# Optimization experiments

Measured on AMD Instinct MI355X. Metric: run time of the kernel, lower is better.

Reference implementation:

```python
import jax, jax.numpy as jnp
import numpy as np

RAD2DEG = 180.0 / 3.14159  # module uses 3.14159, not pi

def _conv2d(x, w):
    # x: (N,1,H,W), w: (O,1,3,3), SAME padding, stride 1
    return jax.lax.conv_general_dilated(
        x, w, window_strides=(1, 1), padding='SAME',
        dimension_numbers=('NCHW', 'OIHW', 'NCHW'))

def _make_filters():
    sobel = np.array([[1, 0, -1], [2, 0, -2], [1, 0, -1]], dtype=np.float32)
    f0   = [[0,0,0],[0,1,-1],[0,0,0]]
    f45  = [[0,0,0],[0,1,0],[0,0,-1]]
    f90  = [[0,0,0],[0,1,0],[0,-1,0]]
    f135 = [[0,0,0],[0,1,0],[-1,0,0]]
    f180 = [[0,0,0],[-1,1,0],[0,0,0]]
    f225 = [[-1,0,0],[0,1,0],[0,0,0]]
    f270 = [[0,-1,0],[0,1,0],[0,0,0]]
    f315 = [[0,0,-1],[0,1,0],[0,0,0]]
    dirs = np.stack([f0,f45,f90,f135,f180,f225,f270,f315]).astype(np.float32)
    return sobel, dirs

def setup_inputs() -> dict:
    key = jax.random.key(0)
    H, W = 2160, 3840
    img = jax.random.uniform(key, (1, 3, H, W), dtype=jnp.float32)
    sobel, dirs = _make_filters()
    sobel_h = jnp.asarray(sobel)[None, None]          # (1,1,3,3)
    sobel_v = jnp.asarray(sobel.T)[None, None]        # (1,1,3,3)
    dir_w = jnp.asarray(dirs)[:, None]                # (8,1,3,3)
    return {"img": img, "sobel_h": sobel_h, "sobel_v": sobel_v, "dir_w": dir_w}

def reference(img, sobel_h, sobel_v, dir_w):
    # grayscale: mean of the 3 channels
    gray = (img[:, 0:1] + img[:, 1:2] + img[:, 2:3]) / 3.0        # (1,1,H,W)
    grad_x = _conv2d(gray, sobel_h)
    grad_y = _conv2d(gray, sobel_v)
    grad_mag = jnp.sqrt(grad_x ** 2 + grad_y ** 2)                # (1,1,H,W)
    # orientation in degrees, snapped to multiples of 45 (round-half-even, like torch.round)
    ori = jnp.round((jnp.arctan2(grad_y, grad_x) * RAD2DEG + 180.0) / 45.0)
    idx_pos = jnp.mod(ori, 8.0).astype(jnp.int32)                 # (1,1,H,W)
    idx_neg = jnp.mod(ori + 4.0, 8.0).astype(jnp.int32)
    all_filtered = _conv2d(grad_mag, dir_w)                       # (1,8,H,W)
    # per-pixel channel select (the flattened gather in the original)
    pos = jnp.take_along_axis(all_filtered, idx_pos, axis=1)      # (1,1,H,W)
    neg = jnp.take_along_axis(all_filtered, idx_neg, axis=1)
    is_max = jnp.minimum(pos, neg) > 0.0
    # in-place aliasing in the original: thin_edges/early_threshold alias grad_mag,
    # so the final binary map is: is_max AND (grad_mag >= 0.2)
    th = jnp.where(is_max & (grad_mag >= 0.2), 1.0, 0.0).astype(jnp.float32)
    return th
```

## Files before the change

kernel.cpp:

```cpp
#include <hip/hip_runtime.h>
#include <math.h>

#define IMG_W 3840
#define IMG_H 2160
#define OUTW  60
#define R     20
#define GROWS (R + 4)
#define MROWS (R + 2)

#define DXPACK 0x901A
#define DYPACK 0x1A9

#define T1_SLOPE 0.41421317376456f
#define T2_SLOPE 2.41420676743300f
#define SECT_EPS 3.0e-5f

__device__ __noinline__ int slow_sector(float sx, float sy) {
#pragma clang fp contract(off)
    const float RADF = (float)(180.0 / 3.14159);
    float t = atan2f(sy, sx);
    float wv = ((t * RADF) + 180.0f) / 45.0f;
    float ori = rintf(wv);
    float fr = fabsf(wv - ori);
    if (fr > 0.4995f) {
        double td = atan2((double)sy, (double)sx);
        float t2 = (float)td;
        wv = ((t2 * RADF) + 180.0f) / 45.0f;
        ori = rintf(wv);
    }
    return ((int)ori) & 7;
}

__global__ __launch_bounds__(256, 4) void canny_like_kernel(const float* __restrict__ img,
                                                            float* __restrict__ out) {
#pragma clang fp contract(off)
    __shared__ float lds_m[4][4][64];

    const int lane = threadIdx.x;
    const int w    = threadIdx.y;
    const int X0   = (blockIdx.x * 4 + w) * OUTW;
    const int Y0   = blockIdx.y * R;
    const int x    = X0 - 2 + lane;
    const bool xok    = (unsigned)x < (unsigned)IMG_W;
    const int  xc     = min(max(x, 0), IMG_W - 1);
    const bool xmok   = (lane >= 1) && (lane <= 62) && xok;
    const bool xoutok = (lane >= 2) && (lane <= 61);

    const float* im1 = img + (size_t)IMG_W * IMG_H;
    const float* im2 = img + 2 * (size_t)IMG_W * IMG_H;

    float g[GROWS];
#pragma unroll
    for (int k = 0; k < GROWS; ++k) {
        const int  y   = Y0 - 2 + k;
        const bool yok = (unsigned)y < (unsigned)IMG_H;
        const int  yc  = min(max(y, 0), IMG_H - 1);
        const int  o   = yc * IMG_W + xc;
        float c0 = img[o], c1 = im1[o], c2 = im2[o];
        float t = ((c0 + c1) + c2) / 3.0f;
        g[k] = (xok && yok) ? t : 0.0f;
    }

    float* const B = &lds_m[w][0][0];

    float gl[3], gr[3];
    gl[0] = __shfl_up(g[0], 1);  gr[0] = __shfl_down(g[0], 1);
    gl[1] = __shfl_up(g[1], 1);  gr[1] = __shfl_down(g[1], 1);

    float mc_p  = 0.0f;
    int   off_p = 0;

#pragma unroll
    for (int m = 0; m < MROWS; ++m) {
        const int i0 = m % 3, i1 = (m + 1) % 3, i2 = (m + 2) % 3;
        gl[i2] = __shfl_up(g[m + 2], 1);
        gr[i2] = __shfl_down(g[m + 2], 1);

        float a00 = gl[i0], a01 = g[m],     a02 = gr[i0];
        float a10 = gl[i1],                 a12 = gr[i1];
        float a20 = gl[i2], a21 = g[m + 2], a22 = gr[i2];
        float sx = a00;
        sx = sx - a02;
        sx = sx + 2.0f * a10;
        sx = sx - 2.0f * a12;
        sx = sx + a20;
        sx = sx - a22;
        float sy = a00;
        sy = sy + 2.0f * a01;
        sy = sy + a02;
        sy = sy - a20;
        sy = sy - 2.0f * a21;
        sy = sy - a22;
        float magv = sqrtf(sx * sx + sy * sy);

        float ax = fabsf(sx), ay = fabsf(sy);
        float d1 = fmaf(-T1_SLOPE, ax, ay);
        float d2 = fmaf(-T2_SLOPE, ax, ay);
        float sA = ax + ay;
        int dxo, dyo;
        if (__builtin_expect(fabsf(d1) < SECT_EPS * sA || fabsf(d2) < SECT_EPS * sA, 0)) {
            int idx = slow_sector(sx, sy);
            dxo = ((DXPACK >> (2 * idx)) & 3) - 1;
            dyo = ((DYPACK >> (2 * idx)) & 3) - 1;
        } else {
            dxo = (d2 > 0.0f) ? 0 : ((sx > 0.0f) ? -1 : 1);
            dyo = (d1 < 0.0f) ? 0 : ((sy > 0.0f) ? -1 : 1);
        }
        const bool vok = xmok && ((unsigned)(Y0 - 1 + m) < (unsigned)IMG_H);
        float mag  = vok ? magv : 0.0f;
        int   offv = vok ? (dyo * 64 + dxo) : 0;

        B[(m & 3) * 64 + lane] = mag;

        if (m >= 2) {
            const int rp  = ((m - 1) & 3) * 64;
            const int ipp = (rp + lane + off_p) & 255;
            const int ipn = (rp + lane - off_p) & 255;
            float mp = B[ipp];
            float mn = B[ipn];
            float res = (fminf(mc_p - mp, mc_p - mn) > 0.0f && mc_p >= 0.2f) ? 1.0f : 0.0f;
            if (xoutok)
                out[(size_t)(Y0 + m - 2) * IMG_W + x] = res;
        }
        mc_p  = mag;
        off_p = offv;
    }
}

extern "C" void kernel_launch(void* const* d_in, const int* in_sizes, int n_in,
                              void* d_out, int out_size, void* d_ws, size_t ws_size,
                              hipStream_t stream) {
    const float* img = (const float*)d_in[0];
    float* out = (float*)d_out;
    dim3 grid(64 / 4, IMG_H / R);
    dim3 block(64, 4);
    canny_like_kernel<<<grid, block, 0, stream>>>(img, out);
}
```

Baseline: 164.6 us.

## Stream image rows through a rolling 4-row register window with prefetch

Replaces the up-front load of all 24 grayscale rows into registers with a software-pipelined rolling window. Each iteration loads the three channels for row k+3 while computing gray, Sobel and NMS for earlier rows, and the loop is kept rolled in blocks of four. This cuts the large register footprint, which may allow higher occupancy. In exchange, each wave has fewer loads in flight, and a few extra clamped rows past the tile end are loaded and never used.

```diff
diff --git a/kernel.cpp b/kernel.cpp
--- a/kernel.cpp
+++ b/kernel.cpp
@@ -6,7 +6,6 @@
 #define OUTW  60
 #define R     20
 #define GROWS (R + 4)
-#define MROWS (R + 2)
 
 #define DXPACK 0x901A
 #define DYPACK 0x1A9
@@ -31,6 +30,81 @@
     return ((int)ori) & 7;
 }
 
+
+#define LOADROW(kk, cj)                                                        \
+    {                                                                          \
+        const int y_  = Y0 - 2 + (kk);                                         \
+        const int yc_ = min(max(y_, 0), IMG_H - 1);                            \
+        const int o_  = yc_ * IMG_W + xc;                                      \
+        c0[(cj)] = img[o_];                                                    \
+        c1[(cj)] = im1[o_];                                                    \
+        c2[(cj)] = im2[o_];                                                    \
+    }
+
+#define GRAY(kk, j3)                                                           \
+    {                                                                          \
+        const int  y_   = Y0 - 2 + (kk);                                       \
+        const bool yok_ = (unsigned)y_ < (unsigned)IMG_H;                      \
+        float t_  = ((c0[(j3)] + c1[(j3)]) + c2[(j3)]) / 3.0f;                 \
+        float gv_ = (xok && yok_) ? t_ : 0.0f;                                 \
+        g[(j3)]  = gv_;                                                        \
+        gl[(j3)] = __shfl_up(gv_, 1);                                          \
+        gr[(j3)] = __shfl_down(gv_, 1);                                        \
+    }
+
+#define MAGROW(kk, j3, DONMS)                                                  \
+    {                                                                          \
+        const int i0_ = ((j3) + 2) & 3, i1_ = ((j3) + 3) & 3, i2_ = (j3);      \
+        float a00 = gl[i0_], a01 = g[i0_], a02 = gr[i0_];                      \
+        float a10 = gl[i1_],               a12 = gr[i1_];                      \
+        float a20 = gl[i2_], a21 = g[i2_], a22 = gr[i2_];                      \
+        float sx = a00;                                \
+        sx = sx - a02;                                                         \
+        sx = sx + 2.0f * a10;                                                  \
+        sx = sx - 2.0f * a12;                                                  \
+        sx = sx + a20;                                                         \
+        sx = sx - a22;                                                         \
+        float sy = a00;                                                        \
+        sy = sy + 2.0f * a01;                                                  \
+        sy = sy + a02;                                                         \
+        sy = sy - a20;                                                         \
+        sy = sy - 2.0f * a21;                                                  \
+        sy = sy - a22;                                                         \
+        float magv = sqrtf(sx * sx + sy * sy);                                 \
+        float ax = fabsf(sx), ay = fabsf(sy);                                  \
+        float d1 = fmaf(-T1_SLOPE, ax, ay);                                    \
+        float d2 = fmaf(-T2_SLOPE, ax, ay);                                    \
+        float sA = ax + ay;                                                    \
+        int dxo, dyo;                                                          \
+        if (__builtin_expect(fabsf(d1) < SECT_EPS * sA ||                      \
+                             fabsf(d2) < SECT_EPS * sA, 0)) {                  \
+            int idx = slow_sector(sx, sy);                                     \
+            dxo = ((DXPACK >> (2 * idx)) & 3) - 1;                             \
+            dyo = ((DYPACK >> (2 * idx)) & 3) - 1;                             \
+        } else {                                                               \
+            dxo = (d2 > 0.0f) ? 0 : ((sx > 0.0f) ? -1 : 1);                    \
+            dyo = (d1 < 0.0f) ? 0 : ((sy > 0.0f) ? -1 : 1);                    \
+        }                                                                      \
+        const bool vok_ = xmok && ((unsigned)(Y0 - 3 + (kk)) < (unsigned)IMG_H); \
+        float mag_  = vok_ ? magv : 0.0f;                                      \
+        int   offv_ = vok_ ? (dyo * 64 + dxo) : 0;                             \
+        B[(((j3) + 2) & 3) * 64 + lane] = mag_;    \
+        if (DONMS) {                                                           \
+            \
+            const int rp_  = (((j3) + 1) & 3) * 64;                            \
+            const int ipp_ = (rp_ + lane + off_p) & 255;                       \
+            const int ipn_ = (rp_ + lane - off_p) & 255;                       \
+            float mp_ = B[ipp_];                                               \
+            float mn_ = B[ipn_];                                               \
+            float res_ = (fminf(mc_p - mp_, mc_p - mn_) > 0.0f &&              \
+                          mc_p >= 0.2f) ? 1.0f : 0.0f;                         \
+            if (xoutok)                                                        \
+                out[(size_t)(Y0 + (kk) - 4) * IMG_W + x] = res_;               \
+        }                                                                      \
+        mc_p  = mag_;                                                          \
+        off_p = offv_;                                                         \
+    }
+
 __global__ __launch_bounds__(256, 4) void canny_like_kernel(const float* __restrict__ img,
                                                             float* __restrict__ out) {
 #pragma clang fp contract(off)
@@ -49,81 +123,43 @@
     const float* im1 = img + (size_t)IMG_W * IMG_H;
     const float* im2 = img + 2 * (size_t)IMG_W * IMG_H;
 
-    float g[GROWS];
-#pragma unroll
-    for (int k = 0; k < GROWS; ++k) {
-        const int  y   = Y0 - 2 + k;
-        const bool yok = (unsigned)y < (unsigned)IMG_H;
-        const int  yc  = min(max(y, 0), IMG_H - 1);
-        const int  o   = yc * IMG_W + xc;
-        float c0 = img[o], c1 = im1[o], c2 = im2[o];
-        float t = ((c0 + c1) + c2) / 3.0f;
-        g[k] = (xok && yok) ? t : 0.0f;
-    }
-
     float* const B = &lds_m[w][0][0];
 
-    float gl[3], gr[3];
-    gl[0] = __shfl_up(g[0], 1);  gr[0] = __shfl_down(g[0], 1);
-    gl[1] = __shfl_up(g[1], 1);  gr[1] = __shfl_down(g[1], 1);
-
+    float c0[4], c1[4], c2[4];
+    float g[4], gl[4], gr[4];
     float mc_p  = 0.0f;
     int   off_p = 0;
 
-#pragma unroll
-    for (int m = 0; m < MROWS; ++m) {
-        const int i0 = m % 3, i1 = (m + 1) % 3, i2 = (m + 2) % 3;
-        gl[i2] = __shfl_up(g[m + 2], 1);
-        gr[i2] = __shfl_down(g[m + 2], 1);
+    LOADROW(0, 0)
+    LOADROW(1, 1)
+    LOADROW(2, 2)
+    GRAY(0, 0)  LOADROW(3, 3)
+    GRAY(1, 1)  LOADROW(4, 0)
+    GRAY(2, 2)  LOADROW(5, 1)  MAGROW(2, 2, 0)
+    GRAY(3, 3)  LOADROW(6, 2)  MAGROW(3, 3, 0)
 
-        float a00 = gl[i0], a01 = g[m],     a02 = gr[i0];
-        float a10 = gl[i1],                 a12 = gr[i1];
-        float a20 = gl[i2], a21 = g[m + 2], a22 = gr[i2];
-        float sx = a00;
-        sx = sx - a02;
-        sx = sx + 2.0f * a10;
-        sx = sx - 2.0f * a12;
-        sx = sx + a20;
-        sx = sx - a22;
-        float sy = a00;
-        sy = sy + 2.0f * a01;
-        sy = sy + a02;
-        sy = sy - a20;
-        sy = sy - 2.0f * a21;
-        sy = sy - a22;
-        float magv = sqrtf(sx * sx + sy * sy);
-
-        float ax = fabsf(sx), ay = fabsf(sy);
-        float d1 = fmaf(-T1_SLOPE, ax, ay);
-        float d2 = fmaf(-T2_SLOPE, ax, ay);
-        float sA = ax + ay;
-        int dxo, dyo;
-        if (__builtin_expect(fabsf(d1) < SECT_EPS * sA || fabsf(d2) < SECT_EPS * sA, 0)) {
-            int idx = slow_sector(sx, sy);
-            dxo = ((DXPACK >> (2 * idx)) & 3) - 1;
-            dyo = ((DYPACK >> (2 * idx)) & 3) - 1;
-        } else {
-            dxo = (d2 > 0.0f) ? 0 : ((sx > 0.0f) ? -1 : 1);
-            dyo = (d1 < 0.0f) ? 0 : ((sy > 0.0f) ? -1 : 1);
+#pragma clang loop unroll(disable)
+    for (int kb = 4; kb < GROWS; kb += 4) {
+        {   const int k_ = kb + 0;
+            LOADROW(k_ + 3, 3)
+            GRAY(k_, 0)
+            MAGROW(k_, 0, 1)
         }
-        const bool vok = xmok && ((unsigned)(Y0 - 1 + m) < (unsigned)IMG_H);
-        float mag  = vok ? magv : 0.0f;
-        int   offv = vok ? (dyo * 64 + dxo) : 0;
-
-        B[(m & 3) * 64 + lane] = mag;
-
-        if (m >= 2) {
-            const int rp  = ((m - 1) & 3) * 64;
-            const int ipp = (rp + lane + off_p) & 255;
-            const int ipn = (rp + lane - off_p) & 255;
-            float mp = B[ipp];
-            float mn = B[ipn];
-            float res = (fminf(mc_p - mp, mc_p - mn) > 0.0f && mc_p >= 0.2f) ? 1.0f : 0.0f;
-            if (xoutok)
-                out[(size_t)(Y0 + m - 2) * IMG_W + x] = res;
+        {   const int k_ = kb + 1;
+            LOADROW(k_ + 3, 0)
+            GRAY(k_, 1)
+            MAGROW(k_, 1, 1)
         }
-        mc_p  = mag;
-        off_p = offv;
+        {   const int k_ = kb + 2;
+            LOADROW(k_ + 3, 1)
+            GRAY(k_, 2)
+            MAGROW(k_, 2, 1)
+        }
+        {   const int k_ = kb + 3;
+            LOADROW(k_ + 3, 2)
+            GRAY(k_, 3)
+            MAGROW(k_, 3, 1)
+        }
     }
 }
 
```

Result: no change. 166.3 us (+1.1%).
